# Kernel tuning notes

Hardware: AMD Instinct MI355X
Metric: run time of the kernel (lower is better)

Reference implementation:

```python
import jax, jax.numpy as jnp
import numpy as np

N_EVENTS = 4096
TS_SIZE = 1024
N_NEURONS = 64
LAMBDA_HOMEO = 0.25
HOMEO_FLAG = True


def setup_inputs() -> dict:
    key = jax.random.key(0)
    k1, k2 = jax.random.split(key)
    all_ts = jax.random.normal(k1, (N_EVENTS, TS_SIZE), dtype=jnp.float32)
    # torch.nn.init.uniform_(weight, a=0, b=1)
    W = jax.random.uniform(k2, (N_NEURONS, TS_SIZE), dtype=jnp.float32)
    cumhisto = jnp.ones((N_NEURONS,), dtype=jnp.float32)
    return {"all_ts": all_ts, "W": W, "cumhisto": cumhisto, "clustering_flag": 1}


def reference(all_ts, W, cumhisto, clustering_flag):
    n_neurons = W.shape[0]
    if clustering_flag:
        # Sequential online competitive learning: per event, normalize, score,
        # argmax winner, update the winner's codebook row and its histogram.
        def step(carry, ts):
            Wc, hist = carry
            ts = ts / jnp.linalg.norm(ts)
            w_norm = jnp.linalg.norm(Wc, axis=1)          # [n_neurons]
            beta = (Wc @ ts) / w_norm                      # [n_neurons]
            if HOMEO_FLAG:
                gain = jnp.exp(LAMBDA_HOMEO * (1.0 - n_neurons * hist / hist.sum()))
                scores = gain * beta
            else:
                scores = beta
            n_star = jnp.argmax(scores)
            Ck = Wc[n_star]                                # [ts_size]
            alpha = 0.01 / (1.0 + hist[n_star] / 20000.0)
            Wc = Wc.at[n_star].set(Ck + alpha * beta[n_star] * (ts - Ck))
            hist = hist.at[n_star].add(1.0)
            return (Wc, hist), n_star

        (_, _), n_star = jax.lax.scan(step, (W, cumhisto), all_ts)
        return n_star  # [n_events] int winners
    else:
        # NB: original normalizes over dim=0 (the event dim) — faithful to source.
        x = all_ts.reshape(all_ts.shape[0], -1)
        x = x / jnp.linalg.norm(x, axis=0)
        beta = (x @ W.T) / jnp.linalg.norm(W, axis=1)      # [n_events, n_neurons]
        return jnp.argmax(beta, axis=1)
```

## Files before the change

### kernel.cpp

```cpp
#include <hip/hip_runtime.h>
#include <math.h>

#define N_EVENTS 4096
#define TS 1024
#define NN 64
#define BLK 512
#define NBLK (N_EVENTS / BLK)

typedef int v2i __attribute__((ext_vector_type(2)));

template<int CTRL>
__device__ __forceinline__ float dppmov(float x) {
    return __int_as_float(__builtin_amdgcn_mov_dpp(__float_as_int(x), CTRL, 0xF, 0xF, true));
}

#if __has_builtin(__builtin_amdgcn_permlane16_swap) && __has_builtin(__builtin_amdgcn_permlane32_swap)
__device__ __forceinline__ void sswap16(float x, float& a, float& b) {
    v2i r = __builtin_amdgcn_permlane16_swap(__float_as_int(x), __float_as_int(x), false, false);
    a = __int_as_float(r[0]); b = __int_as_float(r[1]);
}
__device__ __forceinline__ void sswap32(float x, float& a, float& b) {
    v2i r = __builtin_amdgcn_permlane32_swap(__float_as_int(x), __float_as_int(x), false, false);
    a = __int_as_float(r[0]); b = __int_as_float(r[1]);
}
#else
__device__ __forceinline__ void sswap16(float x, float& a, float& b) {
    asm("v_mov_b32 %0, %2\n\tv_mov_b32 %1, %2\n\ts_nop 1\n\tv_permlane16_swap_b32 %0, %1"
        : "=&v"(a), "=&v"(b) : "v"(x));
}
__device__ __forceinline__ void sswap32(float x, float& a, float& b) {
    asm("v_mov_b32 %0, %2\n\tv_mov_b32 %1, %2\n\ts_nop 1\n\tv_permlane32_swap_b32 %0, %1"
        : "=&v"(a), "=&v"(b) : "v"(x));
}
#endif

__device__ __forceinline__ float wred_add(float x) {
    x += dppmov<0xB1>(x);
    x += dppmov<0x4E>(x);
    x += dppmov<0x141>(x);
    x += dppmov<0x140>(x);
    { float a, b; sswap16(x, a, b); x = a + b; }
    { float a, b; sswap32(x, a, b); x = a + b; }
    return x;
}
__device__ __forceinline__ float wred_max(float x) {
    x = fmaxf(x, dppmov<0xB1>(x));
    x = fmaxf(x, dppmov<0x4E>(x));
    x = fmaxf(x, dppmov<0x141>(x));
    x = fmaxf(x, dppmov<0x140>(x));
    { float a, b; sswap16(x, a, b); x = fmaxf(a, b); }
    { float a, b; sswap32(x, a, b); x = fmaxf(a, b); }
    return x;
}


__global__ void norms_kernel(const float* __restrict__ all_ts, float* __restrict__ nrm) {
    const int l = threadIdx.x & 63;
    const int wv = threadIdx.x >> 6;
    const int e = blockIdx.x * 4 + wv;
    const float4* src = (const float4*)(all_ts + (size_t)e * TS);
    float s = 0.f;
    #pragma unroll
    for (int c = 0; c < 4; ++c) {
        float4 f = src[64 * c + l];
        s = fmaf(f.x, f.x, fmaf(f.y, f.y, fmaf(f.z, f.z, fmaf(f.w, f.w, s))));
    }
    const float tsn = sqrtf(wred_add(s));
    if (l == 0) nrm[e] = tsn;
}

__global__ void wnorm0_kernel(const float* __restrict__ W, const float* __restrict__ ch,
                              float* __restrict__ wn_g, float* __restrict__ hist_g) {
    const int l = threadIdx.x & 63;
    const int wv = threadIdx.x >> 6;
    const int r = blockIdx.x * 4 + wv;
    const float4* row = (const float4*)(W + (size_t)r * TS);
    float s = 0.f;
    #pragma unroll
    for (int c = 0; c < 4; ++c) {
        float4 f = row[64 * c + l];
        s = fmaf(f.x, f.x, fmaf(f.y, f.y, fmaf(f.z, f.z, fmaf(f.w, f.w, s))));
    }
    const float tot = wred_add(s);
    if (l == 0) wn_g[r] = sqrtf(tot);
    if (blockIdx.x == 0 && threadIdx.x < NN) hist_g[threadIdx.x] = ch[threadIdx.x];
}

__global__ void gtile_kernel(const float* __restrict__ ts, float* __restrict__ Gt) {
    const int tj = blockIdx.x, ti = blockIdx.y, b = blockIdx.z;
    if (tj < ti) return;
    __shared__ float As[32][36];
    __shared__ float Bs[32][36];
    const float* base = ts + (size_t)b * BLK * TS;
    const int tid = threadIdx.x;
    const int ty = tid >> 4, tx = tid & 15;
    const int lr = tid >> 3, lc = (tid & 7) << 2;
    float a00 = 0, a01 = 0, a10 = 0, a11 = 0;
    for (int k0 = 0; k0 < TS; k0 += 32) {
        float4 av = *(const float4*)(base + (size_t)(ti * 32 + lr) * TS + k0 + lc);
        float4 bv = *(const float4*)(base + (size_t)(tj * 32 + lr) * TS + k0 + lc);
        __syncthreads();
        *(float4*)&As[lr][lc] = av;
        *(float4*)&Bs[lr][lc] = bv;
        __syncthreads();
        #pragma unroll
        for (int kk = 0; kk < 32; kk += 4) {
            const float4 x0 = *(const float4*)&As[2 * ty][kk];
            const float4 x1 = *(const float4*)&As[2 * ty + 1][kk];
            const float4 y0 = *(const float4*)&Bs[2 * tx][kk];
            const float4 y1 = *(const float4*)&Bs[2 * tx + 1][kk];
            a00 = fmaf(x0.x, y0.x, fmaf(x0.y, y0.y, fmaf(x0.z, y0.z, fmaf(x0.w, y0.w, a00))));
            a01 = fmaf(x0.x, y1.x, fmaf(x0.y, y1.y, fmaf(x0.z, y1.z, fmaf(x0.w, y1.w, a01))));
            a10 = fmaf(x1.x, y0.x, fmaf(x1.y, y0.y, fmaf(x1.z, y0.z, fmaf(x1.w, y0.w, a10))));
            a11 = fmaf(x1.x, y1.x, fmaf(x1.y, y1.y, fmaf(x1.z, y1.z, fmaf(x1.w, y1.w, a11))));
        }
    }
    float* g = Gt + (size_t)b * BLK * BLK;
    const int i0 = ti * 32 + 2 * ty, j0 = tj * 32 + 2 * tx;
    g[(size_t)i0 * BLK + j0]           = a00;
    g[(size_t)i0 * BLK + j0 + 1]       = a01;
    g[(size_t)(i0 + 1) * BLK + j0]     = a10;
    g[(size_t)(i0 + 1) * BLK + j0 + 1] = a11;
}

__global__ void dgemm_kernel(const float* __restrict__ Wc, const float* __restrict__ tsb,
                             float* __restrict__ D_g) {
    const int tj = blockIdx.x, ti = blockIdx.y;
    __shared__ float As[32][36];
    __shared__ float Bs[32][36];
    const int tid = threadIdx.x;
    const int ty = tid >> 4, tx = tid & 15;
    const int lr = tid >> 3, lc = (tid & 7) << 2;
    float a00 = 0, a01 = 0, a10 = 0, a11 = 0;
    for (int k0 = 0; k0 < TS; k0 += 32) {
        float4 av = *(const float4*)(Wc + (size_t)(ti * 32 + lr) * TS + k0 + lc);
        float4 bv = *(const float4*)(tsb + (size_t)(tj * 32 + lr) * TS + k0 + lc);
        __syncthreads();
        *(float4*)&As[lr][lc] = av;
        *(float4*)&Bs[lr][lc] = bv;
        __syncthreads();
        #pragma unroll
        for (int kk = 0; kk < 32; kk += 4) {
            const float4 x0 = *(const float4*)&As[2 * ty][kk];
            const float4 x1 = *(const float4*)&As[2 * ty + 1][kk];
            const float4 y0 = *(const float4*)&Bs[2 * tx][kk];
            const float4 y1 = *(const float4*)&Bs[2 * tx + 1][kk];
            a00 = fmaf(x0.x, y0.x, fmaf(x0.y, y0.y, fmaf(x0.z, y0.z, fmaf(x0.w, y0.w, a00))));
            a01 = fmaf(x0.x, y1.x, fmaf(x0.y, y1.y, fmaf(x0.z, y1.z, fmaf(x0.w, y1.w, a01))));
            a10 = fmaf(x1.x, y0.x, fmaf(x1.y, y0.y, fmaf(x1.z, y0.z, fmaf(x1.w, y0.w, a10))));
            a11 = fmaf(x1.x, y1.x, fmaf(x1.y, y1.y, fmaf(x1.z, y1.z, fmaf(x1.w, y1.w, a11))));
        }
    }
    const int n0 = ti * 32 + 2 * ty, f0 = tj * 32 + 2 * tx;
    D_g[(size_t)n0 * BLK + f0]           = a00;
    D_g[(size_t)n0 * BLK + f0 + 1]       = a01;
    D_g[(size_t)(n0 + 1) * BLK + f0]     = a10;
    D_g[(size_t)(n0 + 1) * BLK + f0 + 1] = a11;
}

__global__ void rebuild_kernel(float* __restrict__ Wc, const float* __restrict__ ts,
                               const int* __restrict__ win, const float* __restrict__ coef_g,
                               const float* __restrict__ nrm, int b) {
    const int n = blockIdx.x;
    const int d = blockIdx.y * 256 + threadIdx.x;
    float wv = Wc[(size_t)n * TS + d];
    const int e0 = b * BLK;
    #pragma unroll 1
    for (int i = 0; i < BLK; ++i) {
        if (win[e0 + i] == n) {
            const float rtn = __builtin_amdgcn_rcpf(nrm[e0 + i]);
            const float tn = ts[(size_t)(e0 + i) * TS + d] * rtn;
            const float c = coef_g[e0 + i];
            wv = fmaf(c, tn - wv, wv);
        }
    }
    Wc[(size_t)n * TS + d] = wv;
}

#define DIDX(n, f) (((n) << 9) + ((f) ^ ((n) & 31)))

#define SEQSTEP(I, G)                                                           \
    {                                                                           \
        const float Dv = Dl[DIDX(l, (I))];                                      \
        const float tsn = nrm[e0 + (I)];                                        \
        const float rtn = __builtin_amdgcn_rcpf(tsn);                           \
        const float beta = Dv * __builtin_amdgcn_rcpf(tsn * wnl);               \
        const float score = gain * beta;                                        \
        const float smax = wred_max(score);                                     \
        const unsigned long long mk = __ballot(score == smax);                  \
        const int ns = (int)(__ffsll(mk) - 1);                                  \
        const float coefl = (0.01f * __builtin_amdgcn_rcpf(1.0f + hll * (1.0f / 20000.0f))) * beta; \
        const float coef = __shfl(coefl, ns, 64);                               \
        if (t == 0) { out[e0 + (I)] = ns; coef_g[e0 + (I)] = coef; }            \
        const float bw = __shfl(beta, ns, 64);                                  \
        if (l == ns) {                                                          \
            const float om = 1.0f - coef;                                       \
            wnl = sqrtf(om * om * wnl * wnl + 2.0f * coef * om * bw * wnl + coef * coef); \
            hll += 1.0f;                                                        \
        }                                                                       \
        hist_sum += 1.0f;                                                       \
        gain = __expf(0.25f - 16.0f * hll * __builtin_amdgcn_rcpf(hist_sum));   \
        if (t > (I)) {                                                          \
            const int a = DIDX(ns, t);                                          \
            const float dv = Dl[a];                                             \
            Dl[a] = fmaf(coef, rtn * (G) - dv, dv);                             \
        }                                                                       \
        if ((I) + 2 < BLK) (G) = Gt_b[((I) + 2) * BLK + t];                     \
        __syncthreads();                                                        \
    }

__launch_bounds__(512, 1)
__global__ void seq_kernel(const float* __restrict__ D_g, const float* __restrict__ Gt_b,
                           const float* __restrict__ nrm, float* __restrict__ wn_g,
                           float* __restrict__ hist_g, int* __restrict__ out,
                           float* __restrict__ coef_g, int b)
{
    __shared__ float Dl[NN * BLK];
    const int t = threadIdx.x;
    const int w = t >> 6;
    const int l = t & 63;

    for (int n0 = 0; n0 < NN; n0 += 4) {
        const int rr = n0 + (t >> 7);
        const int c4 = (t & 127) << 2;
        const float4 dv = *(const float4*)(D_g + (size_t)rr * BLK + c4);
        Dl[DIDX(rr, c4 + 0)] = dv.x;
        Dl[DIDX(rr, c4 + 1)] = dv.y;
        Dl[DIDX(rr, c4 + 2)] = dv.z;
        Dl[DIDX(rr, c4 + 3)] = dv.w;
    }
    float wnl = wn_g[l];
    float hll = hist_g[l];
    float hist_sum = 64.0f + (float)(BLK * b);
    float gain = __expf(0.25f - 16.0f * hll * __builtin_amdgcn_rcpf(hist_sum));
    float g0 = Gt_b[t];
    float g1 = Gt_b[BLK + t];
    const int e0 = b * BLK;
    __syncthreads();

    #pragma unroll 1
    for (int i = 0; i < BLK; i += 2) {
        SEQSTEP(i, g0);
        SEQSTEP(i + 1, g1);
    }

    if (w == 0) { wn_g[l] = wnl; hist_g[l] = hll; }
}

#define NRM_OFF   0
#define WN_OFF    4096
#define HIST_OFF  4160
#define COEF_OFF  4224
#define D_OFF     8320
#define W_OFF     41088
#define GT_OFF    106624

extern "C" void kernel_launch(void* const* d_in, const int* in_sizes, int n_in,
                              void* d_out, int out_size, void* d_ws, size_t ws_size,
                              hipStream_t stream) {
    const float* all_ts   = (const float*)d_in[0];
    const float* W        = (const float*)d_in[1];
    const float* cumhisto = (const float*)d_in[2];
    int* out = (int*)d_out;
    float* ws = (float*)d_ws;

    float* nrm    = ws + NRM_OFF;
    float* wn_g   = ws + WN_OFF;
    float* hist_g = ws + HIST_OFF;
    float* coef_g = ws + COEF_OFF;
    float* D_g    = ws + D_OFF;
    float* W_cur  = ws + W_OFF;
    float* Gt     = ws + GT_OFF;

    hipMemcpyAsync(W_cur, W, (size_t)NN * TS * sizeof(float),
                   hipMemcpyDeviceToDevice, stream);
    norms_kernel<<<N_EVENTS / 4, 256, 0, stream>>>(all_ts, nrm);
    wnorm0_kernel<<<16, 256, 0, stream>>>(W, cumhisto, wn_g, hist_g);
    gtile_kernel<<<dim3(16, 16, NBLK), 256, 0, stream>>>(all_ts, Gt);

    for (int b = 0; b < NBLK; ++b) {
        dgemm_kernel<<<dim3(16, 2), 256, 0, stream>>>(
            W_cur, all_ts + (size_t)b * BLK * TS, D_g);
        seq_kernel<<<1, 512, 0, stream>>>(
            D_g, Gt + (size_t)b * BLK * BLK, nrm, wn_g, hist_g, out, coef_g, b);
        if (b < NBLK - 1)
            rebuild_kernel<<<dim3(NN, 4), 256, 0, stream>>>(
                W_cur, all_ts, out, coef_g, nrm, b);
    }
}
```

Before: 2.493 ms.

## Run sequential winner loop in a single wavefront without block barriers

The sequential scan kernel drops from 512 threads to a single 64-lane wavefront, which removes the per-event __syncthreads. The D tile is stored transposed and swizzled (event-major) so each lane can read its neuron's score with one LDS access. Each lane now applies the winner-row update to 8 future events, using clamped addresses into a dump slot instead of branches. The next event's D value, norm and Gram diagonal are prefetched, and the alpha computation moves off the critical path. The cost is that each lane does more LDS work and holds more registers, and the workspace layout is reordered.

```diff
diff --git a/kernel.cpp b/kernel.cpp
--- a/kernel.cpp
+++ b/kernel.cpp
@@ -152,10 +152,10 @@
         }
     }
     const int n0 = ti * 32 + 2 * ty, f0 = tj * 32 + 2 * tx;
-    D_g[(size_t)n0 * BLK + f0]           = a00;
-    D_g[(size_t)n0 * BLK + f0 + 1]       = a01;
-    D_g[(size_t)(n0 + 1) * BLK + f0]     = a10;
-    D_g[(size_t)(n0 + 1) * BLK + f0 + 1] = a11;
+    D_g[(size_t)f0 * 64       + ((n0)     ^ (f0 & 31))]       = a00;
+    D_g[(size_t)(f0 + 1) * 64 + ((n0)     ^ ((f0 + 1) & 31))] = a01;
+    D_g[(size_t)f0 * 64       + ((n0 + 1) ^ (f0 & 31))]       = a10;
+    D_g[(size_t)(f0 + 1) * 64 + ((n0 + 1) ^ ((f0 + 1) & 31))] = a11;
 }
 
 __global__ void rebuild_kernel(float* __restrict__ Wc, const float* __restrict__ ts,
@@ -177,83 +177,113 @@
     Wc[(size_t)n * TS + d] = wv;
 }
 
-#define DIDX(n, f) (((n) << 9) + ((f) ^ ((n) & 31)))
-
-#define SEQSTEP(I, G)                                                           \
+#define DUMPB 131072u
+
+#define STEP(I, GC, TSC, SDC)                                                   \
     {                                                                           \
-        const float Dv = Dl[DIDX(l, (I))];                                      \
-        const float tsn = nrm[e0 + (I)];                                        \
-        const float rtn = __builtin_amdgcn_rcpf(tsn);                           \
-        const float beta = Dv * __builtin_amdgcn_rcpf(tsn * wnl);               \
+        const float tsn = TSC;                                                  \
+        const float sd  = SDC;                                                  \
+        TSC = nrm[e0 + (I) + 2];                     \
+        SDC = Gt_b[513 * ((I) + 2) + 1];                                        \
+        const float rtn  = __builtin_amdgcn_rcpf(tsn);                          \
+        const float beta = dv * __builtin_amdgcn_rcpf(tsn * wnl);               \
         const float score = gain * beta;                                        \
+        const float coefl = alpha * beta;                                       \
+                   \
+        const float dv_pre = Dl[((((I) + 1) & 511) << 6) + (l ^ (((I) + 1) & 31))]; \
         const float smax = wred_max(score);                                     \
         const unsigned long long mk = __ballot(score == smax);                  \
         const int ns = (int)(__ffsll(mk) - 1);                                  \
-        const float coefl = (0.01f * __builtin_amdgcn_rcpf(1.0f + hll * (1.0f / 20000.0f))) * beta; \
         const float coef = __shfl(coefl, ns, 64);                               \
-        if (t == 0) { out[e0 + (I)] = ns; coef_g[e0 + (I)] = coef; }            \
-        const float bw = __shfl(beta, ns, 64);                                  \
-        if (l == ns) {                                                          \
-            const float om = 1.0f - coef;                                       \
-            wnl = sqrtf(om * om * wnl * wnl + 2.0f * coef * om * bw * wnl + coef * coef); \
-            hll += 1.0f;                                                        \
+        const float bw   = __shfl(beta,  ns, 64);                               \
+        if (l == 0) { out[e0 + (I)] = ns; coef_g[e0 + (I)] = coef; }            \
+              \
+        {                                                                       \
+            const unsigned f0u = (unsigned)((I) + 1 + l);                       \
+            const unsigned fb = (f0u << 8) + (((unsigned)ns ^ (f0u & 31u)) << 2); \
+            const unsigned dmp = DUMPB + ((unsigned)l << 2);                    \
+            _Pragma("unroll")                                                   \
+            for (int k = 0; k < 8; ++k) {                                       \
+                unsigned a = fb + 16384u * (unsigned)k;                         \
+                a = a < dmp ? a : dmp;                                          \
+                float* p = (float*)((char*)Dl + a);                             \
+                const float dvv = *p;                                           \
+                *p = fmaf(coef, rtn * GC[k] - dvv, dvv);                        \
+            }                                                                   \
         }                                                                       \
-        hist_sum += 1.0f;                                                       \
-        gain = __expf(0.25f - 16.0f * hll * __builtin_amdgcn_rcpf(hist_sum));   \
-        if (t > (I)) {                                                          \
-            const int a = DIDX(ns, t);                                          \
-            const float dv = Dl[a];                                             \
-            Dl[a] = fmaf(coef, rtn * (G) - dv, dv);                             \
+                                  \
+        {                                                                       \
+            const float* gr = Gt_b + 512 * ((I) + 2) + ((I) + 3 + l);           \
+            _Pragma("unroll")                                                   \
+            for (int k = 0; k < 8; ++k) GC[k] = gr[64 * k];                     \
         }                                                                       \
-        if ((I) + 2 < BLK) (G) = Gt_b[((I) + 2) * BLK + t];                     \
-        __syncthreads();                                                        \
-    }
-
-__launch_bounds__(512, 1)
+             \
+        const float fx = fmaf(coef, rtn * sd - dv_pre, dv_pre);                 \
+        dv = (l == ns) ? fx : dv_pre;                                           \
+        const float om = 1.0f - coef;                                           \
+        const float wn_new = sqrtf(om * om * wnl * wnl                          \
+                                   + 2.0f * coef * om * bw * wnl + coef * coef); \
+        if (l == ns) { wnl = wn_new; hll += 1.0f; }                             \
+        hs += 1.0f;                                                             \
+        gain  = __expf(0.25f - 16.0f * hll * __builtin_amdgcn_rcpf(hs));        \
+        alpha = 0.01f * __builtin_amdgcn_rcpf(fmaf(hll, 1.0f / 20000.0f, 1.0f)); \
+    }
+
+__launch_bounds__(64, 1)
 __global__ void seq_kernel(const float* __restrict__ D_g, const float* __restrict__ Gt_b,
                            const float* __restrict__ nrm, float* __restrict__ wn_g,
                            float* __restrict__ hist_g, int* __restrict__ out,
                            float* __restrict__ coef_g, int b)
 {
-    __shared__ float Dl[NN * BLK];
-    const int t = threadIdx.x;
-    const int w = t >> 6;
-    const int l = t & 63;
-
-    for (int n0 = 0; n0 < NN; n0 += 4) {
-        const int rr = n0 + (t >> 7);
-        const int c4 = (t & 127) << 2;
-        const float4 dv = *(const float4*)(D_g + (size_t)rr * BLK + c4);
-        Dl[DIDX(rr, c4 + 0)] = dv.x;
-        Dl[DIDX(rr, c4 + 1)] = dv.y;
-        Dl[DIDX(rr, c4 + 2)] = dv.z;
-        Dl[DIDX(rr, c4 + 3)] = dv.w;
-    }
+    __shared__ float Dl[NN * BLK + 64];
+    const int l = threadIdx.x;
+
+    {
+        const float4* Dg4 = (const float4*)D_g;
+        float4* Dl4 = (float4*)Dl;
+        #pragma unroll 8
+        for (int c = 0; c < 128; ++c) Dl4[c * 64 + l] = Dg4[c * 64 + l];
+    }
+
+    const int e0 = b * BLK;
     float wnl = wn_g[l];
     float hll = hist_g[l];
-    float hist_sum = 64.0f + (float)(BLK * b);
-    float gain = __expf(0.25f - 16.0f * hll * __builtin_amdgcn_rcpf(hist_sum));
-    float g0 = Gt_b[t];
-    float g1 = Gt_b[BLK + t];
-    const int e0 = b * BLK;
-    __syncthreads();
+    float hs  = 64.0f + (float)e0;
+    float gain  = __expf(0.25f - 16.0f * hll * __builtin_amdgcn_rcpf(hs));
+    float alpha = 0.01f * __builtin_amdgcn_rcpf(fmaf(hll, 1.0f / 20000.0f, 1.0f));
+
+    float gA[8], gB[8];
+    {
+        const float* gr = Gt_b + (1 + l);
+        #pragma unroll
+        for (int k = 0; k < 8; ++k) gA[k] = gr[64 * k];
+    }
+    {
+        const float* gr = Gt_b + 512 + (2 + l);
+        #pragma unroll
+        for (int k = 0; k < 8; ++k) gB[k] = gr[64 * k];
+    }
+    float tsA = nrm[e0], tsB = nrm[e0 + 1];
+    float sdA = Gt_b[1], sdB = Gt_b[513 + 1];
+    float dv = Dl[l];
 
     #pragma unroll 1
     for (int i = 0; i < BLK; i += 2) {
-        SEQSTEP(i, g0);
-        SEQSTEP(i + 1, g1);
-    }
-
-    if (w == 0) { wn_g[l] = wnl; hist_g[l] = hll; }
-}
-
-#define NRM_OFF   0
-#define WN_OFF    4096
-#define HIST_OFF  4160
-#define COEF_OFF  4224
-#define D_OFF     8320
-#define W_OFF     41088
-#define GT_OFF    106624
+        STEP(i,     gA, tsA, sdA);
+        STEP(i + 1, gB, tsB, sdB);
+    }
+
+    wn_g[l] = wnl;
+    hist_g[l] = hll;
+}
+
+#define GT_OFF    0
+#define NRM_OFF   2097152
+#define WN_OFF    2101248
+#define HIST_OFF  2101312
+#define COEF_OFF  2101376
+#define D_OFF     2105472
+#define W_OFF     2138240
 
 extern "C" void kernel_launch(void* const* d_in, const int* in_sizes, int n_in,
                               void* d_out, int out_size, void* d_ws, size_t ws_size,
@@ -264,13 +294,13 @@
     int* out = (int*)d_out;
     float* ws = (float*)d_ws;
 
+    float* Gt     = ws + GT_OFF;
     float* nrm    = ws + NRM_OFF;
     float* wn_g   = ws + WN_OFF;
     float* hist_g = ws + HIST_OFF;
     float* coef_g = ws + COEF_OFF;
     float* D_g    = ws + D_OFF;
     float* W_cur  = ws + W_OFF;
-    float* Gt     = ws + GT_OFF;
 
     hipMemcpyAsync(W_cur, W, (size_t)NN * TS * sizeof(float),
                    hipMemcpyDeviceToDevice, stream);
@@ -281,7 +311,7 @@
     for (int b = 0; b < NBLK; ++b) {
         dgemm_kernel<<<dim3(16, 2), 256, 0, stream>>>(
             W_cur, all_ts + (size_t)b * BLK * TS, D_g);
-        seq_kernel<<<1, 512, 0, stream>>>(
+        seq_kernel<<<1, 64, 0, stream>>>(
             D_g, Gt + (size_t)b * BLK * BLK, nrm, wn_g, hist_g, out, coef_g, b);
         if (b < NBLK - 1)
             rebuild_kernel<<<dim3(NN, 4), 256, 0, stream>>>(
```

New measurement: 2.922 ms. 17.2% more time.
